# Kernel tuning notes

Hardware: AMD Instinct MI355X
Metric: run time of the kernel (lower is better)

## Reference

```python
import jax, jax.numpy as jnp
import numpy as np

B, S, D_IN, D = 8, 8192, 512, 512  # batch, seq_len, input_dim, dim (dim_inner = dim since expansion=1.0)


def log_g(x):
    # log-space version of g(x) = relu(x)+0.5 for x>=0, sigmoid(x) for x<0
    return jnp.where(x >= 0, jnp.log(jax.nn.relu(x) + 0.5), -jax.nn.softplus(-x))


def heinsen_scan_log(log_coeffs, log_values):
    # parallel linear-recurrence solve in log space
    a_star = jnp.cumsum(log_coeffs, axis=1)                       # [B, S+1, D]
    log_h = a_star + jax.lax.cumlogsumexp(log_values - a_star, axis=1)
    return jnp.exp(log_h)


def setup_inputs() -> dict:
    key = jax.random.key(0)
    k1, k2, k3 = jax.random.split(key, 3)
    x = jax.random.normal(k1, (B, S, D_IN), dtype=jnp.float32)
    prev_hidden = jax.random.normal(k2, (B, D), dtype=jnp.float32)
    W = jax.random.normal(k3, (D_IN, 2 * D), dtype=jnp.float32) / np.sqrt(D_IN)
    return {"x": x, "prev_hidden": prev_hidden, "W": W}


def reference(x, prev_hidden, W):
    seq_len = x.shape[1]
    hidden_gate = jnp.einsum('bsi,id->bsd', x, W)                 # [B, S, 2D]
    hidden, gate = jnp.split(hidden_gate, 2, axis=-1)             # [B, S, D] each
    log_coeffs = -jax.nn.softplus(gate)                           # log(1 - z)
    log_z = -jax.nn.softplus(-gate)                               # log(z)
    log_values = log_z + log_g(hidden)                            # log(z * h_tilde)
    # prepend previous hidden state as step 0 of the recurrence
    log_values = jnp.concatenate([log_g(prev_hidden)[:, None, :], log_values], axis=1)  # [B, S+1, D]
    log_coeffs = jnp.pad(log_coeffs, ((0, 0), (1, 0), (0, 0)))     # [B, S+1, D]
    h = heinsen_scan_log(log_coeffs, log_values)                  # [B, S+1, D]
    out = h[:, -seq_len:]                                         # [B, S, D]
    return out  # to_out is identity since expansion_factor == 1.0
```

## Files before the change

kernel.cpp:

```cpp
#include <hip/hip_runtime.h>
#include <stdint.h>

#define Bb   8
#define Ss   8192
#define DIN  512
#define Dd   512
#define M_TOT (Bb * Ss)
#define NC   64
#define CL   128

static const size_t CV_OFF  = 0;
static const size_t XS_OFF  = 134217728ull;
static const size_t WT_OFF  = XS_OFF + 67108864ull;
static const size_t AG_OFF  = WT_OFF + 1048576ull;
static const size_t WS_NEED = AG_OFF + 2097152ull;

typedef short  short8 __attribute__((ext_vector_type(8)));
typedef float  f32x4  __attribute__((ext_vector_type(4)));

__device__ __forceinline__ unsigned short bf16_rne(float f) {
  uint32_t u = __float_as_uint(f);
  u += 0x7fffu + ((u >> 16) & 1u);
  return (unsigned short)(u >> 16);
}

__device__ __forceinline__ void gload16(const unsigned short* g, void* l) {
  __builtin_amdgcn_global_load_lds(
      (const __attribute__((address_space(1))) uint32_t*)g,
      (__attribute__((address_space(3))) uint32_t*)l, 16, 0, 0);
}

__global__ void k_prep(const float* __restrict__ x, const float* __restrict__ W,
                       unsigned short* __restrict__ xs, unsigned short* __restrict__ wt) {
  const int bx = blockIdx.x;
  if (bx < 4096) {
    const size_t n4 = (size_t)M_TOT * DIN / 4;
    for (size_t i = (size_t)bx * 256 + threadIdx.x; i < n4; i += (size_t)4096 * 256) {
      float4 v = ((const float4*)x)[i];
      size_t e = i * 4;
      size_t r = e >> 9;
      int    k = (int)(e & 511);
      ushort4 hi;
      unsigned short* hp = (unsigned short*)&hi;
      hp[0] = bf16_rne(v.x); hp[1] = bf16_rne(v.y);
      hp[2] = bf16_rne(v.z); hp[3] = bf16_rne(v.w);
      *(ushort4*)(xs + r * 512 + k) = hi;
    }
  } else {
    const int t0 = (bx - 4096) * 256 + threadIdx.x;
    for (int i = t0; i < 512 * 1024; i += 131072) {
      int k = i >> 10;
      int j = i & 1023;
      float w = W[i];
      int n = (j < 512) ? (32 * (j >> 4) + (j & 15))
                        : (32 * ((j - 512) >> 4) + 16 + ((j - 512) & 15));
      wt[n * 512 + k] = bf16_rne(w);
    }
  }
}

__global__ void __launch_bounds__(256) k_gemm(const unsigned short* __restrict__ xs,
                                              const unsigned short* __restrict__ wt,
                                              uint32_t* __restrict__ cvu,
                                              float2* __restrict__ agg) {
  __shared__ __align__(16) unsigned short As[2][128 * 32];
  __shared__ __align__(16) unsigned short Bsh[2][128 * 32];
  __shared__ float aggC[2][2][2][16];
  __shared__ float aggV[2][2][2][16];

  const int tid  = threadIdx.x;
  const int lane = tid & 63;
  const int wave = tid >> 6;
  const int wr = wave >> 1, wc = wave & 1;

  const int bid = blockIdx.x;
  const int xcd = bid & 7;
  const int j8  = bid >> 3;
  const int mb  = xcd * 64 + (j8 >> 3);
  const int nb  = j8 & 7;
  const int m0 = mb * 128, n0 = nb * 128;

  f32x4 acc[4][4] = {};

  const int trow = tid >> 2;
  const int tks  = 8 * ((tid & 3) ^ ((tid >> 3) & 3));
  const size_t aoff0 = (size_t)(m0 + trow) * 512 + tks;
  const size_t aoff1 = aoff0 + (size_t)64 * 512;
  const size_t boff0 = (size_t)(n0 + trow) * 512 + tks;
  const size_t boff1 = boff0 + (size_t)64 * 512;

  const int ra = (lane & 15) * 32 + 8 * ((lane >> 4) ^ ((lane >> 1) & 3));

#define STAGE(bf, k0) { \
    char* la = (char*)As  + (bf) * 8192 + wave * 1024; \
    char* lb = (char*)Bsh + (bf) * 8192 + wave * 1024; \
    gload16(xs + aoff0 + (k0), la); \
    gload16(xs + aoff1 + (k0), la + 4096); \
    gload16(wt + boff0 + (k0), lb); \
    gload16(wt + boff1 + (k0), lb + 4096); }

#define COMPUTE(bf) { \
    const unsigned short* Ab  = &As[bf][0]; \
    const unsigned short* Bb2 = &Bsh[bf][0]; \
    short8 af[4], bfr[4]; \
    _Pragma("unroll") for (int m = 0; m < 4; ++m) \
      af[m] = *(const short8*)(Ab + (wr * 64 + 16 * m) * 32 + ra); \
    _Pragma("unroll") for (int n = 0; n < 4; ++n) \
      bfr[n] = *(const short8*)(Bb2 + (wc * 64 + 16 * n) * 32 + ra); \
    _Pragma("unroll") for (int m = 0; m < 4; ++m) \
      _Pragma("unroll") for (int n = 0; n < 4; ++n) \
        acc[m][n] = __builtin_amdgcn_mfma_f32_16x16x32_bf16(af[m], bfr[n], acc[m][n], 0, 0, 0); }

  STAGE(0, 0);
  __syncthreads();
  int buf = 0;
  for (int kt = 0; kt < 15; ++kt) {
    STAGE(buf ^ 1, (kt + 1) * 32);
    COMPUTE(buf);
    __syncthreads();
    buf ^= 1;
  }
  COMPUTE(buf);

  const int q     = lane >> 4;
  const int rbase = m0 + wr * 64 + (q << 2);
  const int dbase = nb * 64 + wc * 32 + (lane & 15);

  float CW[2] = {1.f, 1.f};
  float VW[2] = {0.f, 0.f};

#pragma unroll
  for (int m = 0; m < 4; ++m) {
#pragma unroll
    for (int t = 0; t < 2; ++t) {
      float cseg = 1.f, vseg = 0.f;
#pragma unroll
      for (int j = 0; j < 4; ++j) {
        float hid = acc[m][2 * t][j];
        float gat = acc[m][2 * t + 1][j];
        float eg = __expf(gat);
        float c  = 1.f / (1.f + eg);
        float z  = 1.f - c;
        float gv = (hid >= 0.f) ? (hid + 0.5f) : (1.f / (1.f + __expf(-hid)));
        float v  = z * gv;
        int R = rbase + 16 * m + j;
        int d = dbase + 16 * t;
        cvu[(size_t)R * 512 + d] =
            (uint32_t)bf16_rne(c) | ((uint32_t)bf16_rne(v) << 16);
        vseg = fmaf(c, vseg, v);
        cseg *= c;
      }
      {
        float Cp = __shfl_xor(cseg, 16);
        float Vp = __shfl_xor(vseg, 16);
        if (q & 1) { vseg = fmaf(cseg, Vp, vseg); cseg = Cp * cseg; }
        else       { vseg = fmaf(Cp, vseg, Vp);   cseg = cseg * Cp; }
        Cp = __shfl_xor(cseg, 32);
        Vp = __shfl_xor(vseg, 32);
        if (q & 2) { vseg = fmaf(cseg, Vp, vseg); cseg = Cp * cseg; }
        else       { vseg = fmaf(Cp, vseg, Vp);   cseg = cseg * Cp; }
      }
      VW[t] = fmaf(cseg, VW[t], vseg);
      CW[t] *= cseg;
    }
  }

  if (lane < 16) {
#pragma unroll
    for (int t = 0; t < 2; ++t) {
      aggC[wr][wc][t][lane] = CW[t];
      aggV[wr][wc][t][lane] = VW[t];
    }
  }
  __syncthreads();
  if (wr == 0 && lane < 16) {
#pragma unroll
    for (int t = 0; t < 2; ++t) {
      float C1 = aggC[1][wc][t][lane];
      float V1 = aggV[1][wc][t][lane];
      int d = nb * 64 + wc * 32 + t * 16 + lane;
      agg[(size_t)mb * 512 + d] = make_float2(CW[t] * C1, fmaf(C1, VW[t], V1));
    }
  }
}

__global__ void k_scan_out(const uint32_t* __restrict__ cvu,
                           const float* __restrict__ prev,
                           const float2* __restrict__ agg,
                           float* __restrict__ out) {
  const int bid   = blockIdx.x;
  const int dh    = bid & 1;
  const int chunk = (bid >> 1) & 63;
  const int b     = bid >> 7;
  const int d     = dh * 256 + threadIdx.x;

  float p = prev[b * 512 + d];
  float h = (p >= 0.f) ? (p + 0.5f) : (1.f / (1.f + __expf(-p)));

  const float2* ag = agg + (size_t)(b * NC) * 512 + d;
#pragma unroll 4
  for (int k = 0; k < chunk; ++k) {
    float2 a = ag[(size_t)k * 512];
    h = fmaf(a.x, h, a.y);
  }

  const size_t base = ((size_t)(b * Ss + chunk * CL)) * 512 + d;
#pragma unroll 8
  for (int i = 0; i < CL; ++i) {
    uint32_t t = __builtin_nontemporal_load(cvu + base + (size_t)i * 512);
    float c = __uint_as_float(t << 16);
    float v = __uint_as_float(t & 0xFFFF0000u);
    h = fmaf(c, h, v);
    __builtin_nontemporal_store(h, out + base + (size_t)i * 512);
  }
}

extern "C" void kernel_launch(void* const* d_in, const int* in_sizes, int n_in,
                              void* d_out, int out_size, void* d_ws, size_t ws_size,
                              hipStream_t stream) {
  if (ws_size < WS_NEED) return;

  const float* x    = (const float*)d_in[0];
  const float* prev = (const float*)d_in[1];
  const float* W    = (const float*)d_in[2];
  float* out = (float*)d_out;
  char* ws = (char*)d_ws;

  uint32_t*       cvu = (uint32_t*)(ws + CV_OFF);
  unsigned short* xs  = (unsigned short*)(ws + XS_OFF);
  unsigned short* wt  = (unsigned short*)(ws + WT_OFF);
  float2*         agg = (float2*)(ws + AG_OFF);

  k_prep<<<dim3(4608), dim3(256), 0, stream>>>(x, W, xs, wt);
  k_gemm<<<dim3(4096), dim3(256), 0, stream>>>(xs, wt, cvu, agg);
  k_scan_out<<<dim3(1024), dim3(256), 0, stream>>>(cvu, prev, agg, out);
}
```

Measured before the change: 367.6 us.

## Fuse x bf16 conversion into GEMM A-tile staging, drop separate xs buffer

The GEMM now reads fp32 x directly into registers, converts it to bf16 with packed hardware conversion, and writes it into LDS, replacing the earlier prep pass that wrote a bf16 copy of x to workspace. This removes one full read and write of a 64 MB intermediate and a kernel's worth of traffic. The epilogue also uses hardware reciprocal and packed bf16 conversion instead of divisions and manual rounding. The A path gives up the async global-to-LDS load, so register pressure rises and more of the load latency is exposed, and each GEMM block now reads twice as many bytes of x.

```diff
diff --git a/kernel.cpp b/kernel.cpp
--- a/kernel.cpp
+++ b/kernel.cpp
@@ -10,8 +10,7 @@
 #define CL   128
 
 static const size_t CV_OFF  = 0;
-static const size_t XS_OFF  = 134217728ull;
-static const size_t WT_OFF  = XS_OFF + 67108864ull;
+static const size_t WT_OFF  = 134217728ull;
 static const size_t AG_OFF  = WT_OFF + 1048576ull;
 static const size_t WS_NEED = AG_OFF + 2097152ull;
 
@@ -30,36 +29,24 @@
       (__attribute__((address_space(3))) uint32_t*)l, 16, 0, 0);
 }
 
-__global__ void k_prep(const float* __restrict__ x, const float* __restrict__ W,
-                       unsigned short* __restrict__ xs, unsigned short* __restrict__ wt) {
-  const int bx = blockIdx.x;
-  if (bx < 4096) {
-    const size_t n4 = (size_t)M_TOT * DIN / 4;
-    for (size_t i = (size_t)bx * 256 + threadIdx.x; i < n4; i += (size_t)4096 * 256) {
-      float4 v = ((const float4*)x)[i];
-      size_t e = i * 4;
-      size_t r = e >> 9;
-      int    k = (int)(e & 511);
-      ushort4 hi;
-      unsigned short* hp = (unsigned short*)&hi;
-      hp[0] = bf16_rne(v.x); hp[1] = bf16_rne(v.y);
-      hp[2] = bf16_rne(v.z); hp[3] = bf16_rne(v.w);
-      *(ushort4*)(xs + r * 512 + k) = hi;
-    }
-  } else {
-    const int t0 = (bx - 4096) * 256 + threadIdx.x;
-    for (int i = t0; i < 512 * 1024; i += 131072) {
-      int k = i >> 10;
-      int j = i & 1023;
-      float w = W[i];
-      int n = (j < 512) ? (32 * (j >> 4) + (j & 15))
-                        : (32 * ((j - 512) >> 4) + 16 + ((j - 512) & 15));
-      wt[n * 512 + k] = bf16_rne(w);
-    }
-  }
-}
-
-__global__ void __launch_bounds__(256) k_gemm(const unsigned short* __restrict__ xs,
+__device__ __forceinline__ uint32_t cvt_pk_bf16(float lo, float hi) {
+  uint32_t r;
+  asm("v_cvt_pk_bf16_f32 %0, %1, %2" : "=v"(r) : "v"(lo), "v"(hi));
+  return r;
+}
+
+__global__ void k_prep_wt(const float* __restrict__ W, unsigned short* __restrict__ wt) {
+  for (int i = blockIdx.x * 256 + threadIdx.x; i < 512 * 1024; i += 512 * 256) {
+    int k = i >> 10;
+    int j = i & 1023;
+    float w = W[i];
+    int n = (j < 512) ? (32 * (j >> 4) + (j & 15))
+                      : (32 * ((j - 512) >> 4) + 16 + ((j - 512) & 15));
+    wt[n * 512 + k] = bf16_rne(w);
+  }
+}
+
+__global__ void __launch_bounds__(256) k_gemm(const float* __restrict__ x,
                                               const unsigned short* __restrict__ wt,
                                               uint32_t* __restrict__ cvu,
                                               float2* __restrict__ agg) {
@@ -84,18 +71,33 @@
 
   const int trow = tid >> 2;
   const int tks  = 8 * ((tid & 3) ^ ((tid >> 3) & 3));
-  const size_t aoff0 = (size_t)(m0 + trow) * 512 + tks;
-  const size_t aoff1 = aoff0 + (size_t)64 * 512;
-  const size_t boff0 = (size_t)(n0 + trow) * 512 + tks;
-  const size_t boff1 = boff0 + (size_t)64 * 512;
+  const size_t axoff0 = (size_t)(m0 + trow) * 512 + tks;
+  const size_t axoff1 = axoff0 + (size_t)64 * 512;
+  const size_t boff0  = (size_t)(n0 + trow) * 512 + tks;
+  const size_t boff1  = boff0 + (size_t)64 * 512;
 
   const int ra = (lane & 15) * 32 + 8 * ((lane >> 4) ^ ((lane >> 1) & 3));
 
-#define STAGE(bf, k0) { \
-    char* la = (char*)As  + (bf) * 8192 + wave * 1024; \
+  float4 sa0, sa1, sa2, sa3;
+
+#define ALOAD(k0) { \
+    const float* p0 = x + axoff0 + (k0); \
+    const float* p1 = x + axoff1 + (k0); \
+    sa0 = *(const float4*)p0; sa1 = *(const float4*)(p0 + 4); \
+    sa2 = *(const float4*)p1; sa3 = *(const float4*)(p1 + 4); }
+
+#define AWRITE(bf) { \
+    uint4 q0, q1; \
+    q0.x = cvt_pk_bf16(sa0.x, sa0.y); q0.y = cvt_pk_bf16(sa0.z, sa0.w); \
+    q0.z = cvt_pk_bf16(sa1.x, sa1.y); q0.w = cvt_pk_bf16(sa1.z, sa1.w); \
+    q1.x = cvt_pk_bf16(sa2.x, sa2.y); q1.y = cvt_pk_bf16(sa2.z, sa2.w); \
+    q1.z = cvt_pk_bf16(sa3.x, sa3.y); q1.w = cvt_pk_bf16(sa3.z, sa3.w); \
+    char* la = (char*)As + (bf) * 8192 + tid * 16; \
+    *(uint4*)la = q0; \
+    *(uint4*)(la + 4096) = q1; }
+
+#define BSTAGE(bf, k0) { \
     char* lb = (char*)Bsh + (bf) * 8192 + wave * 1024; \
-    gload16(xs + aoff0 + (k0), la); \
-    gload16(xs + aoff1 + (k0), la + 4096); \
     gload16(wt + boff0 + (k0), lb); \
     gload16(wt + boff1 + (k0), lb + 4096); }
 
@@ -111,12 +113,17 @@
       _Pragma("unroll") for (int n = 0; n < 4; ++n) \
         acc[m][n] = __builtin_amdgcn_mfma_f32_16x16x32_bf16(af[m], bfr[n], acc[m][n], 0, 0, 0); }
 
-  STAGE(0, 0);
+  ALOAD(0);
+  BSTAGE(0, 0);
+  AWRITE(0);
   __syncthreads();
+
   int buf = 0;
   for (int kt = 0; kt < 15; ++kt) {
-    STAGE(buf ^ 1, (kt + 1) * 32);
+    ALOAD((kt + 1) * 32);
+    BSTAGE(buf ^ 1, (kt + 1) * 32);
     COMPUTE(buf);
+    AWRITE(buf ^ 1);
     __syncthreads();
     buf ^= 1;
   }
@@ -138,15 +145,14 @@
       for (int j = 0; j < 4; ++j) {
         float hid = acc[m][2 * t][j];
         float gat = acc[m][2 * t + 1][j];
-        float eg = __expf(gat);
-        float c  = 1.f / (1.f + eg);
+        float c  = __builtin_amdgcn_rcpf(1.f + __expf(gat));
         float z  = 1.f - c;
-        float gv = (hid >= 0.f) ? (hid + 0.5f) : (1.f / (1.f + __expf(-hid)));
+        float sg = __builtin_amdgcn_rcpf(1.f + __expf(-hid));
+        float gv = (hid >= 0.f) ? (hid + 0.5f) : sg;
         float v  = z * gv;
         int R = rbase + 16 * m + j;
         int d = dbase + 16 * t;
-        cvu[(size_t)R * 512 + d] =
-            (uint32_t)bf16_rne(c) | ((uint32_t)bf16_rne(v) << 16);
+        cvu[(size_t)R * 512 + d] = cvt_pk_bf16(c, v);
         vseg = fmaf(c, vseg, v);
         cseg *= c;
       }
@@ -227,11 +233,10 @@
   char* ws = (char*)d_ws;
 
   uint32_t*       cvu = (uint32_t*)(ws + CV_OFF);
-  unsigned short* xs  = (unsigned short*)(ws + XS_OFF);
   unsigned short* wt  = (unsigned short*)(ws + WT_OFF);
   float2*         agg = (float2*)(ws + AG_OFF);
 
-  k_prep<<<dim3(4608), dim3(256), 0, stream>>>(x, W, xs, wt);
-  k_gemm<<<dim3(4096), dim3(256), 0, stream>>>(xs, wt, cvu, agg);
+  k_prep_wt<<<dim3(512), dim3(256), 0, stream>>>(W, wt);
+  k_gemm<<<dim3(4096), dim3(256), 0, stream>>>(x, wt, cvu, agg);
   k_scan_out<<<dim3(1024), dim3(256), 0, stream>>>(cvu, prev, agg, out);
 }
```

Result: slower. 396.9 us (+7.9%).
